# Kernel optimization log

Hardware: AMD Instinct MI355X
Metric: run time of the kernel (lower is better)

The kernel has to match this reference:

```python
import math
import jax, jax.numpy as jnp
import numpy as np

B, S, D = 2, 1024, 4096
H, DH = 32, 128


def setup_inputs() -> dict:
    key = jax.random.key(0)
    ks = jax.random.split(key, 8)
    scale = 1.0 / math.sqrt(D)
    return {
        "hidden_q": jax.random.normal(ks[0], (B, S, D), jnp.float32),
        "hidden_kv": jax.random.normal(ks[1], (B, S, D), jnp.float32),
        "attention_mask": jax.random.randint(ks[2], (B, S, S), 0, 2) > 0,
        "position_bias": jax.random.normal(ks[3], (B, H, S, S), jnp.float32),
        "Wq": jax.random.normal(ks[4], (D, H * DH), jnp.float32) * scale,
        "Wk": jax.random.normal(ks[5], (D, H * DH), jnp.float32) * scale,
        "Wv": jax.random.normal(ks[6], (D, H * DH), jnp.float32) * scale,
        "Wo": jax.random.normal(ks[7], (H * DH, D), jnp.float32) * scale,
    }


def reference(hidden_q, hidden_kv, attention_mask, position_bias, Wq, Wk, Wv, Wo):
    b, len_q, _ = hidden_q.shape
    len_k = hidden_kv.shape[1]
    # projections -> [B, H, S, DH]
    q = (hidden_q @ Wq).reshape(b, len_q, H, DH).transpose(0, 2, 1, 3)
    k = (hidden_kv @ Wk).reshape(b, len_k, H, DH).transpose(0, 2, 1, 3)
    v = (hidden_kv @ Wv).reshape(b, len_k, H, DH).transpose(0, 2, 1, 3)
    # scores [B, H, Q, K]
    score = jnp.einsum("bhqd,bhkd->bhqk", q, k) / math.sqrt(DH)
    score = score + position_bias
    mask = attention_mask[:, None, :, :]  # [B,1,Q,K]
    score = jnp.where(mask, score, -jnp.inf)
    probs = jax.nn.softmax(score, axis=-1)
    probs = jnp.where(mask, probs, 0.0)  # post-softmax mask (also kills NaN rows)
    ctx = jnp.einsum("bhqk,bhkd->bhqd", probs, v)
    ctx = ctx.transpose(0, 2, 1, 3).reshape(b, len_q, H * DH)
    out = ctx @ Wo
    return out
```

## Files before the change

### kernel.cpp

```cpp
#include <hip/hip_runtime.h>
#include <stdint.h>


#define B_  2
#define S_  1024
#define D_  4096
#define H_  32
#define DH_ 128
#define M_  (B_ * S_)
#define KSTR 8192

typedef __attribute__((ext_vector_type(8))) short bf16x8;
typedef __attribute__((ext_vector_type(4))) float f32x4;

static __device__ __forceinline__ unsigned short f32_to_bf16(float f) {
    unsigned int x = __float_as_uint(f);
    x += 0x7fffu + ((x >> 16) & 1u);
    return (unsigned short)(x >> 16);
}

static __device__ __forceinline__ f32x4 mfma16(bf16x8 a, bf16x8 b, f32x4 c) {
    return __builtin_amdgcn_mfma_f32_16x16x32_bf16(a, b, c, 0, 0, 0);
}

#if defined(__has_builtin)
#if __has_builtin(__builtin_amdgcn_global_load_lds)
#define HAVE_GLOAD_LDS 1
#endif
#endif

#ifdef HAVE_GLOAD_LDS
#define GLD16(g, lbase, lane)                                                  \
    __builtin_amdgcn_global_load_lds(                                          \
        (const __attribute__((address_space(1))) void*)(g),                    \
        (__attribute__((address_space(3))) void*)(lbase), 16, 0, 0)
#else
#define GLD16(g, lbase, lane)                                                  \
    do { *(bf16x8*)((unsigned short*)(lbase) + (size_t)(lane) * 8) =           \
             *(const bf16x8*)(g); } while (0)
#endif

__global__ void detect_mask_kernel(const unsigned char* __restrict__ m, int* flag) {
    int l = threadIdx.x;
    uint4 v = ((const uint4*)m)[l];
    unsigned int ww[4] = {v.x, v.y, v.z, v.w};
    int nz_hi = 0, nz_lo01 = 0;
#pragma unroll
    for (int wi = 0; wi < 4; ++wi)
#pragma unroll
        for (int bi = 0; bi < 4; ++bi) {
            unsigned int byte = (ww[wi] >> (bi * 8)) & 0xffu;
            if (byte && bi != 0) nz_hi = 1;
            if (byte && bi <= 1) nz_lo01 = 1;
        }
    int any_hi = __any(nz_hi);
    int any_lo01 = __any(nz_lo01);
    if (l == 0) *flag = (!any_hi) ? 1 : ((!any_lo01) ? 2 : 0);
}

__global__ void canon_mask_kernel(const void* __restrict__ m, const int* __restrict__ flag,
                                  unsigned char* __restrict__ out, int n) {
    int i = blockIdx.x * 256 + threadIdx.x;
    if (i >= n) return;
    int f = *flag;
    unsigned char v;
    if (f == 1)      v = (unsigned char)(((const int*)m)[i] != 0);
    else if (f == 2) v = (unsigned char)(((const float*)m)[i] != 0.0f);
    else             v = (unsigned char)(((const unsigned char*)m)[i] != 0);
    out[i] = v;
}

__global__ void cvt2_bf16_kernel(const float* __restrict__ a, const float* __restrict__ b,
                                 unsigned short* __restrict__ oa, unsigned short* __restrict__ ob) {
    int i = blockIdx.x * 256 + threadIdx.x;
    const int n4 = (B_ * S_ * D_) / 4;
    const float* src = (i < n4) ? a : b;
    unsigned short* dst = (i < n4) ? oa : ob;
    int j = (i < n4) ? i : i - n4;
    float4 v = ((const float4*)src)[j];
    ushort4 o;
    o.x = f32_to_bf16(v.x); o.y = f32_to_bf16(v.y);
    o.z = f32_to_bf16(v.z); o.w = f32_to_bf16(v.w);
    ((ushort4*)dst)[j] = o;
}

__global__ __launch_bounds__(256) void transpose_all_kernel(
        const float* __restrict__ Wq, const float* __restrict__ Wk,
        const float* __restrict__ Wv, const float* __restrict__ Wo,
        unsigned short* __restrict__ WTq, unsigned short* __restrict__ WTkv,
        unsigned short* __restrict__ WTo) {
    __shared__ unsigned short lds[64][65];
    int which = blockIdx.x >> 12;
    int bid = blockIdx.x & 4095;
    const float* W = (which == 0) ? Wq : (which == 1) ? Wk : (which == 2) ? Wv : Wo;
    unsigned short* WT = (which == 0) ? WTq
                       : (which == 1) ? WTkv
                       : (which == 2) ? (WTkv + (size_t)4096 * 4096)
                                      : WTo;
    int bx = bid & 63;
    int by = bid >> 6;
    int t = threadIdx.x;
    int tr = t >> 4;
    int tc = (t & 15) * 4;
#pragma unroll
    for (int p = 0; p < 4; ++p) {
        int r = p * 16 + tr;
        float4 v = *(const float4*)(W + (size_t)(by * 64 + r) * D_ + bx * 64 + tc);
        lds[r][tc + 0] = f32_to_bf16(v.x);
        lds[r][tc + 1] = f32_to_bf16(v.y);
        lds[r][tc + 2] = f32_to_bf16(v.z);
        lds[r][tc + 3] = f32_to_bf16(v.w);
    }
    __syncthreads();
#pragma unroll
    for (int p = 0; p < 4; ++p) {
        int n = p * 16 + tr;
        ushort4 o;
        o.x = lds[tc + 0][n]; o.y = lds[tc + 1][n];
        o.z = lds[tc + 2][n]; o.w = lds[tc + 3][n];
        *(ushort4*)(WT + (size_t)(bx * 64 + n) * D_ + by * 64 + tc) = o;
    }
}

__global__ __launch_bounds__(256) void vt_kernel(const unsigned short* __restrict__ KV,
                                                 unsigned short* __restrict__ Vtw) {
    __shared__ unsigned short lds[64][72];
    int bid = blockIdx.x;
    int dt = bid & 1;
    int st = (bid >> 1) & 15;
    int h  = (bid >> 5) & 31;
    int b  = bid >> 10;
    int t = threadIdx.x;
    int r = t >> 2;
    int c0 = (t & 3) * 16;
    const unsigned short* src =
        KV + (size_t)(b * S_ + st * 64 + r) * KSTR + 4096 + h * DH_ + dt * 64 + c0;
    bf16x8 v0 = *(const bf16x8*)(src);
    bf16x8 v1 = *(const bf16x8*)(src + 8);
    *(bf16x8*)&lds[r][c0] = v0;
    *(bf16x8*)&lds[r][c0 + 8] = v1;
    __syncthreads();
    unsigned short tmp[16];
#pragma unroll
    for (int i = 0; i < 16; ++i) tmp[i] = lds[c0 + i][r];
    unsigned short* dst =
        Vtw + ((size_t)((b * H_ + h) * DH_ + dt * 64 + r)) * S_ + st * 64 + c0;
    *(bf16x8*)dst = *(bf16x8*)&tmp[0];
    *(bf16x8*)(dst + 8) = *(bf16x8*)&tmp[8];
}

__device__ __forceinline__ void gemm_core(const unsigned short* __restrict__ A,
                                          const unsigned short* __restrict__ BT,
                                          void* __restrict__ C, int out_f32,
                                          int m0, int n0, int cstride,
                                          int koff, int NT, char* ldsc) {
    const int t = threadIdx.x;
    const int w = t >> 6, l = t & 63;
    const int lr = l & 15, lg = l >> 4;
    const int wmh = w >> 2;
    const int walf = w & 3;
    const int wm = wmh << 7;
    const int wn = walf << 6;

    const int ca0 = lg ^ (lr & 7);
    const int aoff0 = lr * 128 + (ca0 << 4);
    const int aoff1 = lr * 128 + ((ca0 ^ 4) << 4);
    const int boff0 = ((walf & 1) * 64 + lr) * 128 + (ca0 << 4);
    const int boff1 = ((walf & 1) * 64 + lr) * 128 + ((ca0 ^ 4) << 4);

    const int srow = t >> 3;
    const int sch = (t & 7) ^ (srow & 7);
    const size_t soff0 = (size_t)srow * 4096 + (size_t)(sch << 3);
    const size_t soff1 = soff0 + (size_t)64 * 4096;
    const int ldso = w << 10;

    f32x4 ac[8][4];
    f32x4 vzero = {0.f, 0.f, 0.f, 0.f};
#pragma unroll
    for (int i = 0; i < 8; ++i)
#pragma unroll
        for (int j = 0; j < 4; ++j) ac[i][j] = vzero;

#define STAGE_ELEM(E, SS)                                                      \
    do {                                                                       \
        int er_ = (E) & 3;                                                     \
        const unsigned short* mb_ = (er_ < 2)                                  \
            ? A + (size_t)(m0 + ((er_ & 1) << 7)) * 4096                       \
            : BT + (size_t)(n0 + ((er_ & 1) << 7)) * 4096;                     \
        mb_ += (size_t)((((E) >> 2) << 6) + koff);                             \
        char* d0_ = ldsc + (SS) * 16384 + ldso;                                \
        GLD16(mb_ + soff0, d0_, l);                                            \
        GLD16(mb_ + soff1, d0_ + 8192, l);                                     \
    } while (0)

#pragma unroll
    for (int e = 0; e < 5; ++e) STAGE_ELEM(e, e);

    const int NT4 = NT << 2;
    int E = 5, ss = 5, s0 = 0;
    bf16x8 bfr[4][2];

#pragma unroll 1
    for (int tau = 0; tau < NT; ++tau) {
        int sA = s0 + wmh;          if (sA >= 9) sA -= 9;
        int sB = s0 + 2 + (walf >> 1); if (sB >= 9) sB -= 9;
        const char* pA0 = ldsc + sA * 16384 + aoff0;
        const char* pA1 = ldsc + sA * 16384 + aoff1;
        const char* pB0 = ldsc + sB * 16384 + boff0;
        const char* pB1 = ldsc + sB * 16384 + boff1;
#pragma unroll
        for (int r = 0; r < 4; ++r) {
            if (r == 0) {
                if (tau == NT - 1)
                    asm volatile("s_waitcnt vmcnt(0)" ::: "memory");
                else
                    asm volatile("s_waitcnt vmcnt(2)" ::: "memory");
            }
            __builtin_amdgcn_s_barrier();
            asm volatile("" ::: "memory");
            if (r == 0) {
#pragma unroll
                for (int nf = 0; nf < 4; ++nf) {
                    bfr[nf][0] = *(const bf16x8*)(pB0 + nf * 2048);
                    bfr[nf][1] = *(const bf16x8*)(pB1 + nf * 2048);
                }
            }
            bf16x8 af[2][2];
            int mfb = r << 1;
#pragma unroll
            for (int j = 0; j < 2; ++j) {
                af[j][0] = *(const bf16x8*)(pA0 + (mfb + j) * 2048);
                af[j][1] = *(const bf16x8*)(pA1 + (mfb + j) * 2048);
            }
            if (E < NT4) STAGE_ELEM(E, ss);
            ++E; ss = (ss == 8) ? 0 : ss + 1;
            __builtin_amdgcn_s_setprio(1);
#pragma unroll
            for (int j = 0; j < 2; ++j)
#pragma unroll
                for (int nf = 0; nf < 4; ++nf) {
                    ac[mfb + j][nf] = mfma16(af[j][0], bfr[nf][0], ac[mfb + j][nf]);
                    ac[mfb + j][nf] = mfma16(af[j][1], bfr[nf][1], ac[mfb + j][nf]);
                }
            __builtin_amdgcn_s_setprio(0);
        }
        s0 += 4; if (s0 >= 9) s0 -= 9;
    }
#undef STAGE_ELEM

#pragma unroll
    for (int mf = 0; mf < 8; ++mf)
#pragma unroll
        for (int nf = 0; nf < 4; ++nf)
#pragma unroll
            for (int q = 0; q < 4; ++q) {
                int row = m0 + wm + mf * 16 + lg * 4 + q;
                int col = n0 + wn + nf * 16 + lr;
                if (out_f32)
                    ((float*)C)[(size_t)row * cstride + col] = ac[mf][nf][q];
                else
                    ((unsigned short*)C)[(size_t)row * cstride + col] = f32_to_bf16(ac[mf][nf][q]);
            }
}

__global__ __launch_bounds__(512, 2) void gemm_qkv_kernel(
        const unsigned short* __restrict__ Aq, const unsigned short* __restrict__ Bq,
        unsigned short* __restrict__ Cq,
        const unsigned short* __restrict__ Akv, const unsigned short* __restrict__ Bkv,
        unsigned short* __restrict__ Ckv) {
    __shared__ char ldsbuf[9 * 16384];
    int bid = blockIdx.x;
    int newid = (bid & 7) * 48 + (bid >> 3);
    if (newid < 128) {
        int bm = newid >> 4, bn = newid & 15;
        gemm_core(Aq, Bq, Cq, 0, bm << 8, bn << 8, 4096, 0, 64, ldsbuf);
    } else {
        int e = newid - 128;
        int bm = e >> 5, bn = e & 31;
        gemm_core(Akv, Bkv, Ckv, 0, bm << 8, bn << 8, 8192, 0, 64, ldsbuf);
    }
}

__global__ __launch_bounds__(512, 2) void gemm_o_kernel(
        const unsigned short* __restrict__ A, const unsigned short* __restrict__ BT,
        float* __restrict__ P) {
    __shared__ char ldsbuf[9 * 16384];
    int bid = blockIdx.x;
    int newid = (bid & 7) * 32 + (bid >> 3);
    int ks = newid >> 7;
    int tile = newid & 127;
    int bm = tile >> 4, bn = tile & 15;
    gemm_core(A, BT, P + (size_t)ks * M_ * D_, 1, bm << 8, bn << 8, 4096,
              ks * 2048, 32, ldsbuf);
}

__global__ void reduce_o_kernel(const float* __restrict__ P, float* __restrict__ out) {
    int i = blockIdx.x * 256 + threadIdx.x;
    float4 a = ((const float4*)P)[i];
    float4 b = ((const float4*)(P + (size_t)M_ * D_))[i];
    float4 o; o.x = a.x + b.x; o.y = a.y + b.y; o.z = a.z + b.z; o.w = a.w + b.w;
    ((float4*)out)[i] = o;
}

#define NEGF (-1e30f)
__global__ __launch_bounds__(256, 2) void attn_kernel(const unsigned short* __restrict__ Qw,
                                                      const unsigned short* __restrict__ KV,
                                                      const unsigned short* __restrict__ Vtw,
                                                      const float* __restrict__ bias,
                                                      const unsigned char* __restrict__ maskc,
                                                      unsigned short* __restrict__ ctx) {
    __shared__ unsigned short Kbuf[2][64 * 128];
    __shared__ unsigned short Vbuf[2][128 * 64];
    __shared__ unsigned short Plds[4][16 * 72];

    int bid = blockIdx.x;
    int qt = bid & 15, h = (bid >> 4) & 31, b = bid >> 9;
    int t = threadIdx.x, w = t >> 6, l = t & 63;
    int lr = l & 15, lg = l >> 4;
    int q0 = (qt << 6) + (w << 4);

    bf16x8 qf[4];
    const unsigned short* Qp = Qw + ((size_t)(b * S_ + q0 + lr)) * D_ + h * DH_ + lg * 8;
#pragma unroll
    for (int kf = 0; kf < 4; ++kf) qf[kf] = *(const bf16x8*)(Qp + kf * 32);

    f32x4 o[8];
    f32x4 vzero = {0.f, 0.f, 0.f, 0.f};
#pragma unroll
    for (int i = 0; i < 8; ++i) o[i] = vzero;
    float m_run[4], l_run[4];
#pragma unroll
    for (int r = 0; r < 4; ++r) { m_run[r] = NEGF; l_run[r] = 0.f; }

    const float* biasp = bias + (((size_t)(b * H_ + h)) << 20)
                              + (((size_t)(q0 + (lg << 2))) << 10) + lr;
    const unsigned char* mp = maskc + ((size_t)b << 20)
                              + (((size_t)(q0 + (lg << 2))) << 10) + lr;
    const unsigned short* Kg = KV + (size_t)(b * S_) * KSTR + h * DH_;
    const unsigned short* Vg = Vtw + (((size_t)(b * H_ + h)) * DH_) * S_;

    float br0[16], br1[16];
    int mr0[16], mr1[16];

#define STAGE_KV(KT, BUF)                                                          \
    do { int kv0_ = (KT) << 6;                                                     \
        _Pragma("unroll")                                                          \
        for (int c = 0; c < 4; ++c) {                                              \
            int seg = (w << 2) + c;                                                \
            int krow = (seg << 2) + (l >> 4);                                      \
            int kch = (l & 15) ^ (krow & 7);                                       \
            GLD16(Kg + (size_t)(kv0_ + krow) * KSTR + (kch << 3),                  \
                  &Kbuf[BUF][seg << 9], l);                                        \
            int vrow = (seg << 3) + (l >> 3);                                      \
            int vch = (l & 7) ^ (vrow & 7);                                        \
            GLD16(Vg + (size_t)vrow * S_ + kv0_ + (vch << 3),                      \
                  &Vbuf[BUF][seg << 9], l);                                        \
        }                                                                          \
    } while (0)

#define LOAD_BM(BR, MR, KT)                                                        \
    do { int kv0_ = (KT) << 6;                                                     \
        _Pragma("unroll")                                                          \
        for (int nb = 0; nb < 4; ++nb)                                             \
            _Pragma("unroll")                                                      \
            for (int r = 0; r < 4; ++r) {                                          \
                BR[nb * 4 + r] = biasp[((size_t)r << 10) + kv0_ + (nb << 4)];      \
                MR[nb * 4 + r] = mp[((size_t)r << 10) + kv0_ + (nb << 4)];         \
            }                                                                      \
    } while (0)

#define COMPUTE(BUF, BR, MR)                                                       \
    do {                                                                           \
        f32x4 s_[4];                                                               \
        _Pragma("unroll")                                                          \
        for (int nb = 0; nb < 4; ++nb) {                                           \
            s_[nb] = vzero;                                                        \
            int krow = (nb << 4) + lr;                                             \
            _Pragma("unroll")                                                      \
            for (int kf = 0; kf < 4; ++kf) {                                       \
                int ba = ((krow << 8) + (((kf << 5) + (lg << 3)) << 1))            \
                         ^ ((krow & 7) << 4);                                      \
                bf16x8 kfr = *(const bf16x8*)((const char*)Kbuf[BUF] + ba);        \
                s_[nb] = mfma16(qf[kf], kfr, s_[nb]);                              \
            }                                                                      \
        }                                                                          \
        float sv[4][4];                                                            \
        _Pragma("unroll")                                                          \
        for (int nb = 0; nb < 4; ++nb)                                             \
            _Pragma("unroll")                                                      \
            for (int r = 0; r < 4; ++r) {                                          \
                float x = fmaf(s_[nb][r], 0.08838834764831845f, BR[nb * 4 + r]);   \
                sv[nb][r] = MR[nb * 4 + r] ? x : NEGF;                             \
            }                                                                      \
        float mt[4], al[4], rs[4];                                                 \
        _Pragma("unroll")                                                          \
        for (int r = 0; r < 4; ++r)                                                \
            mt[r] = fmaxf(fmaxf(sv[0][r], sv[1][r]), fmaxf(sv[2][r], sv[3][r]));   \
        _Pragma("unroll")                                                          \
        for (int off = 1; off < 16; off <<= 1)                                     \
            _Pragma("unroll")                                                      \
            for (int r = 0; r < 4; ++r) mt[r] = fmaxf(mt[r], __shfl_xor(mt[r], off, 64)); \
        _Pragma("unroll")                                                          \
        for (int r = 0; r < 4; ++r) {                                              \
            float mn = fmaxf(m_run[r], mt[r]);                                     \
            al[r] = __expf(m_run[r] - mn);                                         \
            m_run[r] = mn;                                                         \
        }                                                                          \
        _Pragma("unroll")                                                          \
        for (int nb = 0; nb < 4; ++nb)                                             \
            _Pragma("unroll")                                                      \
            for (int r = 0; r < 4; ++r) sv[nb][r] = __expf(sv[nb][r] - m_run[r]);  \
        _Pragma("unroll")                                                          \
        for (int r = 0; r < 4; ++r)                                                \
            rs[r] = (sv[0][r] + sv[1][r]) + (sv[2][r] + sv[3][r]);                 \
        _Pragma("unroll")                                                          \
        for (int off = 1; off < 16; off <<= 1)                                     \
            _Pragma("unroll")                                                      \
            for (int r = 0; r < 4; ++r) rs[r] += __shfl_xor(rs[r], off, 64);       \
        _Pragma("unroll")                                                          \
        for (int r = 0; r < 4; ++r) l_run[r] = l_run[r] * al[r] + rs[r];           \
        _Pragma("unroll")                                                          \
        for (int nb2 = 0; nb2 < 8; ++nb2) {                                        \
            o[nb2][0] *= al[0]; o[nb2][1] *= al[1];                                \
            o[nb2][2] *= al[2]; o[nb2][3] *= al[3];                                \
        }                                                                          \
        _Pragma("unroll")                                                          \
        for (int nb = 0; nb < 4; ++nb)                                             \
            _Pragma("unroll")                                                      \
            for (int r = 0; r < 4; ++r)                                            \
                Plds[w][((lg << 2) + r) * 72 + (nb << 4) + lr] = f32_to_bf16(sv[nb][r]); \
        _Pragma("unroll")                                                          \
        for (int kf2 = 0; kf2 < 2; ++kf2) {                                        \
            bf16x8 pf = *(const bf16x8*)&Plds[w][lr * 72 + (kf2 << 5) + (lg << 3)]; \
            _Pragma("unroll")                                                      \
            for (int nb2 = 0; nb2 < 8; ++nb2) {                                    \
                int dh = (nb2 << 4) + lr;                                          \
                int ba = ((dh << 7) + (((kf2 << 5) + (lg << 3)) << 1))             \
                         ^ ((dh & 7) << 4);                                        \
                bf16x8 vf = *(const bf16x8*)((const char*)Vbuf[BUF] + ba);         \
                o[nb2] = mfma16(pf, vf, o[nb2]);                                   \
            }                                                                      \
        }                                                                          \
    } while (0)

    STAGE_KV(0, 0);
    LOAD_BM(br0, mr0, 0);

#pragma unroll 1
    for (int kt = 0; kt < 16; kt += 2) {
        __syncthreads();
        STAGE_KV(kt + 1, 1);
        LOAD_BM(br1, mr1, kt + 1);
        COMPUTE(0, br0, mr0);
        __syncthreads();
        if (kt < 14) {
            STAGE_KV(kt + 2, 0);
            LOAD_BM(br0, mr0, kt + 2);
        }
        COMPUTE(1, br1, mr1);
    }

#pragma unroll
    for (int r = 0; r < 4; ++r) {
        float inv = l_run[r] > 0.f ? 1.0f / l_run[r] : 0.f;
        int q = q0 + (lg << 2) + r;
        unsigned short* cp = ctx + ((size_t)(b * S_ + q)) * D_ + h * DH_ + lr;
#pragma unroll
        for (int nb2 = 0; nb2 < 8; ++nb2)
            cp[nb2 * 16] = f32_to_bf16(o[nb2][r] * inv);
    }
#undef STAGE_KV
#undef LOAD_BM
#undef COMPUTE
}

extern "C" void kernel_launch(void* const* d_in, const int* in_sizes, int n_in,
                              void* d_out, int out_size, void* d_ws, size_t ws_size,
                              hipStream_t stream) {
    const float* hq   = (const float*)d_in[0];
    const float* hkv  = (const float*)d_in[1];
    const void*  mask = d_in[2];
    const float* bias = (const float*)d_in[3];
    const float* Wq   = (const float*)d_in[4];
    const float* Wk   = (const float*)d_in[5];
    const float* Wv   = (const float*)d_in[6];
    const float* Wo   = (const float*)d_in[7];
    float* out = (float*)d_out;

    char* ws = (char*)d_ws;
    unsigned char* mask_c = (unsigned char*)ws;
    int* flag             = (int*)(ws + (2u << 20));
    unsigned short* hq_b  = (unsigned short*)(ws + (2u << 20) + 4096);
    unsigned short* hkv_b = hq_b + ((size_t)1 << 23);
    unsigned short* WTq   = hkv_b + ((size_t)1 << 23);
    unsigned short* WTo   = WTq + ((size_t)1 << 24);
    unsigned short* WTkv  = WTo + ((size_t)1 << 24);
    unsigned short* Qws   = WTkv + ((size_t)1 << 25);
    unsigned short* KVws  = Qws + ((size_t)1 << 23);
    unsigned short* Cws   = KVws + ((size_t)1 << 24);
    unsigned short* Vtw   = Cws + ((size_t)1 << 23);
    float* Pws            = (float*)(Vtw + ((size_t)1 << 23));

    detect_mask_kernel<<<1, 64, 0, stream>>>((const unsigned char*)mask, flag);
    canon_mask_kernel<<<8192, 256, 0, stream>>>(mask, flag, mask_c, B_ * S_ * S_);
    cvt2_bf16_kernel<<<16384, 256, 0, stream>>>(hq, hkv, hq_b, hkv_b);
    transpose_all_kernel<<<16384, 256, 0, stream>>>(Wq, Wk, Wv, Wo, WTq, WTkv, WTo);

    gemm_qkv_kernel<<<384, 512, 0, stream>>>(hq_b, WTq, Qws, hkv_b, WTkv, KVws);

    vt_kernel<<<B_ * H_ * 16 * 2, 256, 0, stream>>>(KVws, Vtw);
    attn_kernel<<<B_ * H_ * (S_ / 64), 256, 0, stream>>>(Qws, KVws, Vtw, bias, mask_c, Cws);

    gemm_o_kernel<<<256, 512, 0, stream>>>(Cws, WTo, Pws);
    reduce_o_kernel<<<(M_ * D_) / 1024, 256, 0, stream>>>(Pws, out);
}
```

Measured before the change: 526.3 us.

## Split-K Q projection, register-staged single-buffer attention with block swizzle

The Q projection GEMM now uses split-K over two halves, writing fp32 partials that a new reduce kernel sums and converts to bf16. This raises the QKV launch from 384 to 512 blocks so the machine is better filled. The attention kernel swaps its double-buffered LDS for one K/V buffer fed through registers, which allows 3 blocks per CU, and it remaps block IDs. The cost is extra fp32 partial traffic, one more kernel launch, and more barriers per attention iteration.

```diff
diff --git a/kernel.cpp b/kernel.cpp
--- a/kernel.cpp
+++ b/kernel.cpp
@@ -265,20 +265,33 @@
 
 __global__ __launch_bounds__(512, 2) void gemm_qkv_kernel(
         const unsigned short* __restrict__ Aq, const unsigned short* __restrict__ Bq,
-        unsigned short* __restrict__ Cq,
+        float* __restrict__ Pq,
         const unsigned short* __restrict__ Akv, const unsigned short* __restrict__ Bkv,
         unsigned short* __restrict__ Ckv) {
     __shared__ char ldsbuf[9 * 16384];
     int bid = blockIdx.x;
-    int newid = (bid & 7) * 48 + (bid >> 3);
-    if (newid < 128) {
-        int bm = newid >> 4, bn = newid & 15;
-        gemm_core(Aq, Bq, Cq, 0, bm << 8, bn << 8, 4096, 0, 64, ldsbuf);
+    int newid = (bid & 7) * 64 + (bid >> 3);
+    if (newid < 256) {
+        int bm = newid >> 5, bn = newid & 31;
+        gemm_core(Akv, Bkv, Ckv, 0, bm << 8, bn << 8, 8192, 0, 64, ldsbuf);
     } else {
-        int e = newid - 128;
-        int bm = e >> 5, bn = e & 31;
-        gemm_core(Akv, Bkv, Ckv, 0, bm << 8, bn << 8, 8192, 0, 64, ldsbuf);
+        int e = newid - 256;
+        int ks = e >> 7;
+        int tile = e & 127;
+        int bm = tile >> 4, bn = tile & 15;
+        gemm_core(Aq, Bq, Pq + (size_t)ks * M_ * D_, 1, bm << 8, bn << 8, 4096,
+                  ks * 2048, 32, ldsbuf);
     }
+}
+
+__global__ void reduce_q_kernel(const float* __restrict__ P, unsigned short* __restrict__ out) {
+    int i = blockIdx.x * 256 + threadIdx.x;
+    float4 a = ((const float4*)P)[i];
+    float4 b = ((const float4*)(P + (size_t)M_ * D_))[i];
+    ushort4 o;
+    o.x = f32_to_bf16(a.x + b.x); o.y = f32_to_bf16(a.y + b.y);
+    o.z = f32_to_bf16(a.z + b.z); o.w = f32_to_bf16(a.w + b.w);
+    ((ushort4*)out)[i] = o;
 }
 
 __global__ __launch_bounds__(512, 2) void gemm_o_kernel(
@@ -303,17 +316,18 @@
 }
 
 #define NEGF (-1e30f)
-__global__ __launch_bounds__(256, 2) void attn_kernel(const unsigned short* __restrict__ Qw,
+__global__ __launch_bounds__(256, 3) void attn_kernel(const unsigned short* __restrict__ Qw,
                                                       const unsigned short* __restrict__ KV,
                                                       const unsigned short* __restrict__ Vtw,
                                                       const float* __restrict__ bias,
                                                       const unsigned char* __restrict__ maskc,
                                                       unsigned short* __restrict__ ctx) {
-    __shared__ unsigned short Kbuf[2][64 * 128];
-    __shared__ unsigned short Vbuf[2][128 * 64];
+    __shared__ unsigned short Kbuf[64 * 128];
+    __shared__ unsigned short Vbuf[128 * 64];
     __shared__ unsigned short Plds[4][16 * 72];
 
-    int bid = blockIdx.x;
+    int bid0 = blockIdx.x;
+    int bid = (bid0 & 7) * 128 + (bid0 >> 3);
     int qt = bid & 15, h = (bid >> 4) & 31, b = bid >> 9;
     int t = threadIdx.x, w = t >> 6, l = t & 63;
     int lr = l & 15, lg = l >> 4;
@@ -339,22 +353,37 @@
     const unsigned short* Kg = KV + (size_t)(b * S_) * KSTR + h * DH_;
     const unsigned short* Vg = Vtw + (((size_t)(b * H_ + h)) * DH_) * S_;
 
+    bf16x8 kreg[4], vreg[4];
     float br0[16], br1[16];
     int mr0[16], mr1[16];
 
-#define STAGE_KV(KT, BUF)                                                          \
+    const int seg0 = (w << 2);
+    const int krow_b = (l >> 4);
+    const int kch_l = (l & 15);
+    const int vrow_b = (l >> 3);
+    const int vch_l = (l & 7);
+
+#define GLOAD(KT)                                                                  \
     do { int kv0_ = (KT) << 6;                                                     \
         _Pragma("unroll")                                                          \
         for (int c = 0; c < 4; ++c) {                                              \
-            int seg = (w << 2) + c;                                                \
-            int krow = (seg << 2) + (l >> 4);                                      \
-            int kch = (l & 15) ^ (krow & 7);                                       \
-            GLD16(Kg + (size_t)(kv0_ + krow) * KSTR + (kch << 3),                  \
-                  &Kbuf[BUF][seg << 9], l);                                        \
-            int vrow = (seg << 3) + (l >> 3);                                      \
-            int vch = (l & 7) ^ (vrow & 7);                                        \
-            GLD16(Vg + (size_t)vrow * S_ + kv0_ + (vch << 3),                      \
-                  &Vbuf[BUF][seg << 9], l);                                        \
+            int seg = seg0 + c;                                                    \
+            int krow = (seg << 2) + krow_b;                                        \
+            int kch = kch_l ^ (krow & 7);                                          \
+            kreg[c] = *(const bf16x8*)(Kg + (size_t)(kv0_ + krow) * KSTR + (kch << 3)); \
+            int vrow = (seg << 3) + vrow_b;                                        \
+            int vch = vch_l ^ (vrow & 7);                                          \
+            vreg[c] = *(const bf16x8*)(Vg + (size_t)vrow * S_ + kv0_ + (vch << 3)); \
+        }                                                                          \
+    } while (0)
+
+#define DSWRITE()                                                                  \
+    do {                                                                           \
+        _Pragma("unroll")                                                          \
+        for (int c = 0; c < 4; ++c) {                                              \
+            int seg = seg0 + c;                                                    \
+            *(bf16x8*)((char*)Kbuf + (seg << 10) + (l << 4)) = kreg[c];            \
+            *(bf16x8*)((char*)Vbuf + (seg << 10) + (l << 4)) = vreg[c];            \
         }                                                                          \
     } while (0)
 
@@ -369,7 +398,7 @@
             }                                                                      \
     } while (0)
 
-#define COMPUTE(BUF, BR, MR)                                                       \
+#define COMPUTE(BR, MR)                                                            \
     do {                                                                           \
         f32x4 s_[4];                                                               \
         _Pragma("unroll")                                                          \
@@ -380,7 +409,7 @@
             for (int kf = 0; kf < 4; ++kf) {                                       \
                 int ba = ((krow << 8) + (((kf << 5) + (lg << 3)) << 1))            \
                          ^ ((krow & 7) << 4);                                      \
-                bf16x8 kfr = *(const bf16x8*)((const char*)Kbuf[BUF] + ba);        \
+                bf16x8 kfr = *(const bf16x8*)((const char*)Kbuf + ba);             \
                 s_[nb] = mfma16(qf[kf], kfr, s_[nb]);                              \
             }                                                                      \
         }                                                                          \
@@ -437,27 +466,32 @@
                 int dh = (nb2 << 4) + lr;                                          \
                 int ba = ((dh << 7) + (((kf2 << 5) + (lg << 3)) << 1))             \
                          ^ ((dh & 7) << 4);                                        \
-                bf16x8 vf = *(const bf16x8*)((const char*)Vbuf[BUF] + ba);         \
+                bf16x8 vf = *(const bf16x8*)((const char*)Vbuf + ba);              \
                 o[nb2] = mfma16(pf, vf, o[nb2]);                                   \
             }                                                                      \
         }                                                                          \
     } while (0)
 
-    STAGE_KV(0, 0);
+    GLOAD(0);
     LOAD_BM(br0, mr0, 0);
 
 #pragma unroll 1
     for (int kt = 0; kt < 16; kt += 2) {
         __syncthreads();
-        STAGE_KV(kt + 1, 1);
+        DSWRITE();
+        GLOAD(kt + 1);
         LOAD_BM(br1, mr1, kt + 1);
-        COMPUTE(0, br0, mr0);
         __syncthreads();
+        COMPUTE(br0, mr0);
+
+        __syncthreads();
+        DSWRITE();
         if (kt < 14) {
-            STAGE_KV(kt + 2, 0);
+            GLOAD(kt + 2);
             LOAD_BM(br0, mr0, kt + 2);
         }
-        COMPUTE(1, br1, mr1);
+        __syncthreads();
+        COMPUTE(br1, mr1);
     }
 
 #pragma unroll
@@ -469,7 +503,8 @@
         for (int nb2 = 0; nb2 < 8; ++nb2)
             cp[nb2 * 16] = f32_to_bf16(o[nb2][r] * inv);
     }
-#undef STAGE_KV
+#undef GLOAD
+#undef DSWRITE
 #undef LOAD_BM
 #undef COMPUTE
 }
@@ -506,7 +541,8 @@
     cvt2_bf16_kernel<<<16384, 256, 0, stream>>>(hq, hkv, hq_b, hkv_b);
     transpose_all_kernel<<<16384, 256, 0, stream>>>(Wq, Wk, Wv, Wo, WTq, WTkv, WTo);
 
-    gemm_qkv_kernel<<<384, 512, 0, stream>>>(hq_b, WTq, Qws, hkv_b, WTkv, KVws);
+    gemm_qkv_kernel<<<512, 512, 0, stream>>>(hq_b, WTq, Pws, hkv_b, WTkv, KVws);
+    reduce_q_kernel<<<(M_ * D_) / 1024, 256, 0, stream>>>(Pws, Qws);
 
     vt_kernel<<<B_ * H_ * 16 * 2, 256, 0, stream>>>(KVws, Vtw);
     attn_kernel<<<B_ * H_ * (S_ / 64), 256, 0, stream>>>(Qws, KVws, Vtw, bias, mask_c, Cws);
```

New measurement: 1.214 ms. 131% more time.
